# Kernel optimization log

Hardware: AMD Instinct MI355X
Metric: run time of the kernel (lower is better)

The kernel has to match this reference:

```python
import jax, jax.numpy as jnp
import numpy as np

K = 5  # per_pix_kernel


def spatial_attention(x, w):
    # x: [N, k^2, H, W]; w: [1, 2, 7, 7] conv weight, padding=3, no bias
    avg = jnp.mean(x, axis=1, keepdims=True)
    mx = jnp.max(x, axis=1, keepdims=True)
    s = jnp.concatenate([avg, mx], axis=1)  # [N,2,H,W]
    y = jax.lax.conv_general_dilated(
        s, w, window_strides=(1, 1), padding=[(3, 3), (3, 3)],
        dimension_numbers=('NCHW', 'OIHW', 'NCHW'))
    return jax.nn.sigmoid(y)  # [N,1,H,W]


def fac(feat, filters, k):
    # feat: [N,C,H,W]; filters: [N,k^2,H,W] per-pixel kernel shared across channels
    N, C, H, W = feat.shape
    pad = (k - 1) // 2
    p = jnp.pad(feat, ((0, 0), (0, 0), (pad, pad), (pad, pad)))
    # patches[n,c,h,w,s] with s = kh*k + kw (matches torch unfold(2).unfold(3) row-major order)
    patches = jnp.stack([p[:, :, i:i + H, j:j + W]
                         for i in range(k) for j in range(k)], axis=-1)
    return jnp.einsum('nchws,nshw->nchw', patches, filters)


def setup_inputs() -> dict:
    key = jax.random.key(0)
    ks = jax.random.split(key, 7)
    N, C, H, W = 16, 3, 256, 256
    return {
        'blur_info': jax.random.normal(ks[0], (N, C, H, W), jnp.float32),
        'perpix_1': jax.random.normal(ks[1], (N, K * K, H, W), jnp.float32),
        'perpix_2': jax.random.normal(ks[2], (N, K * K, H, W), jnp.float32),
        'perpix_3': jax.random.normal(ks[3], (N, K * K, H, W), jnp.float32),
        'w1': jax.random.normal(ks[4], (1, 2, 7, 7), jnp.float32) * 0.1,
        'w2': jax.random.normal(ks[5], (1, 2, 7, 7), jnp.float32) * 0.1,
        'w3': jax.random.normal(ks[6], (1, 2, 7, 7), jnp.float32) * 0.1,
    }


def reference(blur_info, perpix_1, perpix_2, perpix_3, w1, w2, w3):
    perpix = [perpix_1, perpix_2, perpix_3]
    weights = [w1, w2, w3]
    reblur = []
    for pk, w in zip(perpix, weights):
        mask = spatial_attention(pk, w)            # [N,1,H,W]
        sharp = blur_info * (1.0 - mask)
        blur = fac(blur_info * mask, pk, K)        # per-pixel adaptive filtering
        reblur.append(sharp + blur)
    out = reblur[0]
    for r in reblur[1:]:
        out = out + r
    return out / len(reblur)
```

## Files before the change

### kernel.cpp

```cpp
#include <hip/hip_runtime.h>

#define NIMG 16
#define NC 3
#define H 256
#define W 256
#define HW (H * W)
#define NS 25
#define TH 32
#define TW 32
#define SRH (TH + 10)
#define SRW (TW + 10)
#define SRN (SRH * SRW)
#define MRH (TH + 4)
#define MRW (TW + 4)
#define MRN (MRH * MRW)
#define NTHREADS 256
#define PPT ((TH * TW) / NTHREADS)
#define RPT ((SRN + NTHREADS - 1) / NTHREADS)

__device__ __forceinline__ unsigned bf16r(float x) {
    union { float f; unsigned u; } c; c.f = x;
    return (c.u + 0x7FFFu + ((c.u >> 16) & 1u)) >> 16;
}
__device__ __forceinline__ float bf_hi(unsigned u) {
    union { unsigned u; float f; } c; c.u = u & 0xFFFF0000u; return c.f;
}
__device__ __forceinline__ float bf_lo(unsigned u) {
    union { unsigned u; float f; } c; c.u = u << 16; return c.f;
}

__global__ __launch_bounds__(NTHREADS, 4)
void reblur_fused(const float* __restrict__ blur_info,
                  const float* __restrict__ pp0,
                  const float* __restrict__ pp1,
                  const float* __restrict__ pp2,
                  const float* __restrict__ wt0,
                  const float* __restrict__ wt1,
                  const float* __restrict__ wt2,
                  float* __restrict__ out)
{
    __shared__ unsigned s_l[SRN];
    __shared__ float q[NC][MRN];
    __shared__ float wts[3][98];

    const int tid = threadIdx.x;
    const int n  = blockIdx.z;
    const int h0 = blockIdx.y * TH;
    const int w0 = blockIdx.x * TW;

    if (tid < 98) {
        float sc = (tid < 49) ? 0.04f : 1.0f;
        wts[0][tid] = wt0[tid] * sc;
        wts[1][tid] = wt1[tid] * sc;
        wts[2][tid] = wt2[tid] * sc;
    }

    int off[RPT]; bool val[RPT];
    #pragma unroll
    for (int r = 0; r < RPT; ++r) {
        int rp = tid + r * NTHREADS;
        int rr = rp / SRW, cc = rp % SRW;
        int gh = h0 - 5 + rr, gw = w0 - 5 + cc;
        val[r] = (rp < SRN) && ((unsigned)gh < H) && ((unsigned)gw < W);
        off[r] = gh * W + gw;
    }

    float facc0[PPT], facc1[PPT], facc2[PPT];
    #pragma unroll
    for (int k = 0; k < PPT; ++k) { facc0[k] = 0.f; facc1[k] = 0.f; facc2[k] = 0.f; }

    const size_t nbase = (size_t)n * NS * HW;

    #pragma unroll 1
    for (int b = 0; b < 3; ++b) {
        const float* pb = (b == 0) ? pp0 : ((b == 1) ? pp1 : pp2);
        pb += nbase;

        float sm[RPT], mx[RPT];
        #pragma unroll
        for (int r = 0; r < RPT; ++r) { sm[r] = 0.f; mx[r] = -3.0e38f; }
        #pragma unroll 5
        for (int s = 0; s < NS; ++s) {
            const float* pl = pb + s * HW;
            #pragma unroll
            for (int r = 0; r < RPT; ++r) {
                float v = val[r] ? pl[off[r]] : 0.f;
                sm[r] += v;
                mx[r] = fmaxf(mx[r], v);
            }
        }
        #pragma unroll
        for (int r = 0; r < RPT; ++r) {
            int rp = tid + r * NTHREADS;
            if (rp < SRN)
                s_l[rp] = val[r] ? ((bf16r(sm[r]) << 16) | bf16r(mx[r])) : 0u;
        }
        __syncthreads();

        const float* wb = &wts[b][0];
        for (int i = tid; i < MRN; i += NTHREADS) {
            int rr = i / MRW, cc = i % MRW;
            float a = 0.f;
            #pragma unroll
            for (int j = 0; j < 7; ++j) {
                #pragma unroll
                for (int t = 0; t < 7; ++t) {
                    unsigned u = s_l[(rr + j) * SRW + cc + t];
                    a += bf_hi(u) * wb[j * 7 + t] + bf_lo(u) * wb[49 + j * 7 + t];
                }
            }
            float m = 1.f / (1.f + __expf(-a));
            int gh = h0 - 2 + rr, gw = w0 - 2 + cc;
            bool inb = (unsigned)gh < H && (unsigned)gw < W;
            int gi = gh * W + gw;
            #pragma unroll
            for (int c = 0; c < NC; ++c) {
                float bv = inb ? blur_info[(n * NC + c) * HW + gi] : 0.f;
                q[c][i] = m * bv;
            }
        }
        __syncthreads();

        #pragma unroll
        for (int k = 0; k < PPT; ++k) {
            int oi = tid + k * NTHREADS;
            int r = oi / TW, cc = oi % TW;
            const float* pk = pb + (h0 + r) * W + (w0 + cc);
            int qc = (r + 2) * MRW + cc + 2;
            float f0 = -q[0][qc], f1 = -q[1][qc], f2 = -q[2][qc];
            #pragma unroll
            for (int s = 0; s < NS; ++s) {
                int qi = (r + s / 5) * MRW + cc + (s % 5);
                float v = pk[s * HW];
                f0 += v * q[0][qi];
                f1 += v * q[1][qi];
                f2 += v * q[2][qi];
            }
            facc0[k] += f0; facc1[k] += f1; facc2[k] += f2;
        }
    }

    const float inv3 = 1.f / 3.f;
    #pragma unroll
    for (int k = 0; k < PPT; ++k) {
        int oi = tid + k * NTHREADS;
        int r = oi / TW, cc = oi % TW;
        int gi = (h0 + r) * W + (w0 + cc);
        out[(n * NC + 0) * HW + gi] = blur_info[(n * NC + 0) * HW + gi] + facc0[k] * inv3;
        out[(n * NC + 1) * HW + gi] = blur_info[(n * NC + 1) * HW + gi] + facc1[k] * inv3;
        out[(n * NC + 2) * HW + gi] = blur_info[(n * NC + 2) * HW + gi] + facc2[k] * inv3;
    }
}

extern "C" void kernel_launch(void* const* d_in, const int* in_sizes, int n_in,
                              void* d_out, int out_size, void* d_ws, size_t ws_size,
                              hipStream_t stream) {
    const float* blur = (const float*)d_in[0];
    float* out = (float*)d_out;

    dim3 grid(W / TW, H / TH, NIMG);
    reblur_fused<<<grid, NTHREADS, 0, stream>>>(
        blur,
        (const float*)d_in[1], (const float*)d_in[2], (const float*)d_in[3],
        (const float*)d_in[4], (const float*)d_in[5], (const float*)d_in[6],
        out);
}
```

Measured before the change: 419.4 us.

## Keep per-pixel filter taps in registers and remap blocks for XCD locality

Each thread now loads its own pixels' 25 filter taps once, keeps them in registers (100 floats), and reuses them both for the channel mean/max reduction and for the adaptive filtering. Halo pixels are reduced in a separate loop. This removes the second global read of the per-pixel kernels. The block index is also remapped so consecutive blocks, which go to different XCDs, cover neighbouring tiles, and launch bounds drop to 2 waves per SIMD to make room for the extra registers. The trade-off is lower occupancy and an uneven halo workload across threads.

```diff
diff --git a/kernel.cpp b/kernel.cpp
--- a/kernel.cpp
+++ b/kernel.cpp
@@ -16,7 +16,7 @@
 #define MRN (MRH * MRW)
 #define NTHREADS 256
 #define PPT ((TH * TW) / NTHREADS)
-#define RPT ((SRN + NTHREADS - 1) / NTHREADS)
+#define NHALO (SRN - TH * TW)
 
 __device__ __forceinline__ unsigned bf16r(float x) {
     union { float f; unsigned u; } c; c.f = x;
@@ -29,7 +29,7 @@
     union { unsigned u; float f; } c; c.u = u << 16; return c.f;
 }
 
-__global__ __launch_bounds__(NTHREADS, 4)
+__global__ __launch_bounds__(NTHREADS, 2)
 void reblur_fused(const float* __restrict__ blur_info,
                   const float* __restrict__ pp0,
                   const float* __restrict__ pp1,
@@ -44,9 +44,12 @@
     __shared__ float wts[3][98];
 
     const int tid = threadIdx.x;
-    const int n  = blockIdx.z;
-    const int h0 = blockIdx.y * TH;
-    const int w0 = blockIdx.x * TW;
+
+    const int id  = blockIdx.x + (blockIdx.y << 3) + (blockIdx.z << 6);
+    const int sid = ((id & 7) << 7) + (id >> 3);
+    const int n   = sid >> 6;
+    const int h0  = ((sid >> 3) & 7) * TH;
+    const int w0  = (sid & 7) * TW;
 
     if (tid < 98) {
         float sc = (tid < 49) ? 0.04f : 1.0f;
@@ -55,45 +58,56 @@
         wts[2][tid] = wt2[tid] * sc;
     }
 
-    int off[RPT]; bool val[RPT];
-    #pragma unroll
-    for (int r = 0; r < RPT; ++r) {
-        int rp = tid + r * NTHREADS;
-        int rr = rp / SRW, cc = rp % SRW;
-        int gh = h0 - 5 + rr, gw = w0 - 5 + cc;
-        val[r] = (rp < SRN) && ((unsigned)gh < H) && ((unsigned)gw < W);
-        off[r] = gh * W + gw;
-    }
-
     float facc0[PPT], facc1[PPT], facc2[PPT];
     #pragma unroll
     for (int k = 0; k < PPT; ++k) { facc0[k] = 0.f; facc1[k] = 0.f; facc2[k] = 0.f; }
 
     const size_t nbase = (size_t)n * NS * HW;
 
+    float pk[PPT][NS];
+
     #pragma unroll 1
     for (int b = 0; b < 3; ++b) {
         const float* pb = (b == 0) ? pp0 : ((b == 1) ? pp1 : pp2);
         pb += nbase;
 
-        float sm[RPT], mx[RPT];
         #pragma unroll
-        for (int r = 0; r < RPT; ++r) { sm[r] = 0.f; mx[r] = -3.0e38f; }
-        #pragma unroll 5
-        for (int s = 0; s < NS; ++s) {
-            const float* pl = pb + s * HW;
+        for (int k = 0; k < PPT; ++k) {
+            const int oi = tid + k * NTHREADS;
+            const int r = oi >> 5, c = oi & 31;
+            const float* p = pb + (h0 + r) * W + (w0 + c);
+            float v = p[0];
+            pk[k][0] = v;
+            float sm = v, mx = v;
             #pragma unroll
-            for (int r = 0; r < RPT; ++r) {
-                float v = val[r] ? pl[off[r]] : 0.f;
-                sm[r] += v;
-                mx[r] = fmaxf(mx[r], v);
+            for (int s = 1; s < NS; ++s) {
+                v = p[s * HW];
+                pk[k][s] = v;
+                sm += v; mx = fmaxf(mx, v);
             }
+            s_l[(r + 5) * SRW + (c + 5)] = (bf16r(sm) << 16) | bf16r(mx);
         }
-        #pragma unroll
-        for (int r = 0; r < RPT; ++r) {
-            int rp = tid + r * NTHREADS;
-            if (rp < SRN)
-                s_l[rp] = val[r] ? ((bf16r(sm[r]) << 16) | bf16r(mx[r])) : 0u;
+
+        for (int m = tid; m < NHALO; m += NTHREADS) {
+            int rr, cc;
+            if (m < 210)      { rr = m / 42;              cc = m % 42; }
+            else if (m < 420) { int t = m - 210; rr = 37 + t / 42; cc = t % 42; }
+            else              { int t = m - 420; rr = 5 + t / 10;
+                                int c2 = t % 10; cc = (c2 < 5) ? c2 : c2 + 32; }
+            const int gh = h0 - 5 + rr, gw = w0 - 5 + cc;
+            unsigned u = 0;
+            if ((unsigned)gh < H && (unsigned)gw < W) {
+                const float* p = pb + gh * W + gw;
+                float v = p[0];
+                float sm = v, mx = v;
+                #pragma unroll
+                for (int s = 1; s < NS; ++s) {
+                    v = p[s * HW];
+                    sm += v; mx = fmaxf(mx, v);
+                }
+                u = (bf16r(sm) << 16) | bf16r(mx);
+            }
+            s_l[rr * SRW + cc] = u;
         }
         __syncthreads();
 
@@ -123,15 +137,14 @@
 
         #pragma unroll
         for (int k = 0; k < PPT; ++k) {
-            int oi = tid + k * NTHREADS;
-            int r = oi / TW, cc = oi % TW;
-            const float* pk = pb + (h0 + r) * W + (w0 + cc);
-            int qc = (r + 2) * MRW + cc + 2;
+            const int oi = tid + k * NTHREADS;
+            const int r = oi >> 5, c = oi & 31;
+            const int qc = (r + 2) * MRW + c + 2;
             float f0 = -q[0][qc], f1 = -q[1][qc], f2 = -q[2][qc];
             #pragma unroll
             for (int s = 0; s < NS; ++s) {
-                int qi = (r + s / 5) * MRW + cc + (s % 5);
-                float v = pk[s * HW];
+                const int qi = (r + s / 5) * MRW + c + (s % 5);
+                const float v = pk[k][s];
                 f0 += v * q[0][qi];
                 f1 += v * q[1][qi];
                 f2 += v * q[2][qi];
@@ -143,9 +156,9 @@
     const float inv3 = 1.f / 3.f;
     #pragma unroll
     for (int k = 0; k < PPT; ++k) {
-        int oi = tid + k * NTHREADS;
-        int r = oi / TW, cc = oi % TW;
-        int gi = (h0 + r) * W + (w0 + cc);
+        const int oi = tid + k * NTHREADS;
+        const int r = oi >> 5, c = oi & 31;
+        const int gi = (h0 + r) * W + (w0 + c);
         out[(n * NC + 0) * HW + gi] = blur_info[(n * NC + 0) * HW + gi] + facc0[k] * inv3;
         out[(n * NC + 1) * HW + gi] = blur_info[(n * NC + 1) * HW + gi] + facc1[k] * inv3;
         out[(n * NC + 2) * HW + gi] = blur_info[(n * NC + 2) * HW + gi] + facc2[k] * inv3;
```

After: 375.6 us. 10.4% less time.
